# Kernel optimization log

Hardware: AMD Instinct MI355X
Metric: run time of the kernel (lower is better)

The kernel has to match this reference:

```python
import jax, jax.numpy as jnp
import numpy as np

NC = 80          # classes
REG_MAX = 16     # DFL bins
NK = 51          # 17*3 keypoint channels
KPT_SHAPE = (17, 3)
MAX_DET = 100
CONF_THRES = 0.25
STRIDES = (8, 16, 32)


def _conv1x1(f, w, b):
    # f: (B,C,H,W), w: (O,C), b: (O,) -> (B,O,H,W)
    return jnp.einsum('bchw,oc->bohw', f, w) + b[None, :, None, None]


def _make_anchors(shapes, strides, offset=0.5):
    pts, sts = [], []
    for (h, w), s in zip(shapes, strides):
        sx = jnp.arange(w, dtype=jnp.float32) + offset
        sy = jnp.arange(h, dtype=jnp.float32) + offset
        gy, gx = jnp.meshgrid(sy, sx, indexing='ij')
        pts.append(jnp.stack([gx, gy], -1).reshape(-1, 2))
        sts.append(jnp.full((h * w, 1), float(s), jnp.float32))
    # transposed as in _new_inference: anchors (2,A), strides (1,A)
    return jnp.concatenate(pts, 0).T, jnp.concatenate(sts, 0).T


def setup_inputs() -> dict:
    key = jax.random.key(0)
    ks = jax.random.split(key, 16)
    ch = (128, 256, 512)
    hw = ((80, 80), (40, 40), (20, 20))
    d = {}
    for i, (c, (h, w)) in enumerate(zip(ch, hw)):
        d[f'x{i}'] = jax.random.normal(ks[i], (16, c, h, w), jnp.float32)
    k = 3
    for name, oc in (('cv2', 4 * REG_MAX), ('cv3', NC), ('cv4', NK)):
        for i, c in enumerate(ch):
            d[f'{name}_w{i}'] = jax.random.normal(ks[k], (oc, c), jnp.float32) * 0.02
            d[f'{name}_b{i}'] = jnp.zeros((oc,), jnp.float32)
            k += 1
    return d


def reference(x0, x1, x2,
              cv2_w0, cv2_b0, cv2_w1, cv2_b1, cv2_w2, cv2_b2,
              cv3_w0, cv3_b0, cv3_w1, cv3_b1, cv3_w2, cv3_b2,
              cv4_w0, cv4_b0, cv4_w1, cv4_b1, cv4_w2, cv4_b2):
    feats = [x0, x1, x2]
    cv2 = [(cv2_w0, cv2_b0), (cv2_w1, cv2_b1), (cv2_w2, cv2_b2)]
    cv3 = [(cv3_w0, cv3_b0), (cv3_w1, cv3_b1), (cv3_w2, cv3_b2)]
    cv4 = [(cv4_w0, cv4_b0), (cv4_w1, cv4_b1), (cv4_w2, cv4_b2)]
    bs = x0.shape[0]

    # keypoint branch: cat over levels -> (bs, nk, A)
    kpt = jnp.concatenate(
        [_conv1x1(f, w, b).reshape(bs, NK, -1) for f, (w, b) in zip(feats, cv4)], -1)
    # box+cls branch -> (bs, 4*reg_max+nc, A)
    xcat = jnp.concatenate(
        [jnp.concatenate([_conv1x1(f, *cv2[i]), _conv1x1(f, *cv3[i])], 1).reshape(bs, 4 * REG_MAX + NC, -1)
         for i, f in enumerate(feats)], -1)
    box, cls = xcat[:, :4 * REG_MAX], xcat[:, 4 * REG_MAX:]

    shapes = [(f.shape[2], f.shape[3]) for f in feats]
    anchors, strides = _make_anchors(shapes, STRIDES)  # (2,A), (1,A)
    A = anchors.shape[1]

    # DFL decode: softmax over reg_max bins, expectation w/ arange weights
    p = jax.nn.softmax(box.reshape(bs, 4, REG_MAX, A), axis=2)
    dist = jnp.einsum('bfra,r->bfa', p, jnp.arange(REG_MAX, dtype=jnp.float32))
    lt, rb = dist[:, :2], dist[:, 2:]
    x1y1 = anchors[None] - lt
    x2y2 = anchors[None] + rb
    # xywh box coding, scaled by strides
    dbox = jnp.concatenate([(x1y1 + x2y2) * 0.5, x2y2 - x1y1], 1) * strides[None]  # (bs,4,A)

    # keypoint decode (Pose.kpts_decode, ndim==3)
    y = kpt.reshape(bs, KPT_SHAPE[0], KPT_SHAPE[1], A)
    kxy = (y[:, :, :2] * 2.0 + (anchors[None, None] - 0.5)) * strides[None, None]
    kv = jax.nn.sigmoid(y[:, :, 2:3])
    pred_kpts = jnp.concatenate([kxy, kv], 2).reshape(bs, NK, A).transpose(0, 2, 1)  # (bs,A,nk)

    # EfficientIdxNMS_TRT stand-in: sigmoid scores (score_activation=1),
    # class-agnostic deterministic top-k selection by best class score.
    scores = jax.nn.sigmoid(cls.transpose(0, 2, 1))  # (bs,A,nc)
    max_s = scores.max(-1)
    cls_id = jnp.argmax(scores, -1)
    top_s, top_i = jax.lax.top_k(max_s, MAX_DET)     # (bs,MAX_DET)
    num_dets = (top_s > CONF_THRES).sum(-1).astype(jnp.int32)[:, None]
    det_boxes = jnp.take_along_axis(dbox.transpose(0, 2, 1), top_i[..., None], 1)  # (bs,MAX_DET,4)
    det_classes = jnp.take_along_axis(cls_id, top_i, 1).astype(jnp.int32)
    # irregular keypoint gather via det indices (the pred_kpts[bs_indices, det_indices] step)
    det_kpts = jnp.take_along_axis(pred_kpts, top_i[..., None], 1).reshape(bs, MAX_DET, *KPT_SHAPE)
    return num_dets, det_boxes, top_s, det_classes, det_kpts
```

## Files before the change

kernel.cpp:

```cpp
#include <hip/hip_runtime.h>
#include <hip/hip_bf16.h>

#define NC 80
#define NK 51
#define REG_MAX 16
#define MAX_DET 100
#define A_TOT 8400
#define BS 16

#define OUT_NUM 0
#define OUT_BOX 16
#define OUT_SCORE (16 + 16*MAX_DET*4)
#define OUT_CLASS (OUT_SCORE + 16*MAX_DET)
#define OUT_KPT (OUT_CLASS + 16*MAX_DET)

static __device__ __forceinline__ unsigned long long mk_key(unsigned u, int a) {
    return ((unsigned long long)u << 32) | (unsigned)(0x7FFFFFFF - a);
}

__global__ __launch_bounds__(256) void scores_fused(
    const float* __restrict__ x0, const float* __restrict__ x1, const float* __restrict__ x2,
    const float* __restrict__ w0, const float* __restrict__ w1, const float* __restrict__ w2,
    const float* __restrict__ bias0, const float* __restrict__ bias1, const float* __restrict__ bias2,
    float* __restrict__ max_s,
    int* __restrict__ cls_id)
{
    __shared__ float fs[32 * 256];
    __shared__ float wsh[80 * 32];
    __shared__ float rm[4][256];
    __shared__ int   ri[4][256];

    int bid = blockIdx.x;
    const float *x, *w, *bias; int C, A, a_off, b, tile;
    if (bid < 32) {
        x = x2; w = w2; bias = bias2; C = 512; A = 400; a_off = 8000;
        b = bid >> 1; tile = bid & 1;
    } else if (bid < 144) {
        int r = bid - 32;
        x = x1; w = w1; bias = bias1; C = 256; A = 1600; a_off = 6400;
        b = r / 7; tile = r - b * 7;
    } else {
        int r = bid - 144;
        x = x0; w = w0; bias = bias0; C = 128; A = 6400; a_off = 0;
        b = r / 25; tile = r - b * 25;
    }
    int a0 = tile * 256;

    int t = threadIdx.x;
    int lane = t & 63;
    int wv = t >> 6;
    int oc0 = wv * 20;

    float acc[20][4];
#pragma unroll
    for (int j = 0; j < 20; ++j) {
        float bv = bias[oc0 + j];
        acc[j][0] = bv; acc[j][1] = bv; acc[j][2] = bv; acc[j][3] = bv;
    }

    const float* xb = x + (long)b * C * A;
    int nchunk = C >> 5;

    for (int kc = 0; kc < nchunk; ++kc) {
        __syncthreads();
#pragma unroll
        for (int i = 0; i < 8; ++i) {
            int idx = t + i * 256;
            int c = idx >> 6;
            int q = (idx & 63) * 4;
            int aa = a0 + q; if (aa > A - 4) aa = A - 4;
            float4 v = *(const float4*)(xb + (long)(kc * 32 + c) * A + aa);
            *(float4*)(&fs[c * 256 + q]) = v;
        }
#pragma unroll
        for (int i = 0; i < 3; ++i) {
            int idx = t + i * 256;
            if (idx < 640) {
                int oc = idx >> 3;
                int q = (idx & 7) * 4;
                float4 v = *(const float4*)(w + oc * C + kc * 32 + q);
                *(float4*)(&wsh[oc * 32 + q]) = v;
            }
        }
        __syncthreads();

#pragma unroll 1
        for (int c4 = 0; c4 < 32; c4 += 4) {
            float4 f[4];
#pragma unroll
            for (int cc = 0; cc < 4; ++cc)
                f[cc] = *(const float4*)(&fs[(c4 + cc) * 256 + lane * 4]);
#pragma unroll
            for (int j = 0; j < 20; ++j) {
                float4 w4 = *(const float4*)(&wsh[(oc0 + j) * 32 + c4]);
                acc[j][0] = fmaf(w4.x, f[0].x, acc[j][0]);
                acc[j][0] = fmaf(w4.y, f[1].x, acc[j][0]);
                acc[j][0] = fmaf(w4.z, f[2].x, acc[j][0]);
                acc[j][0] = fmaf(w4.w, f[3].x, acc[j][0]);
                acc[j][1] = fmaf(w4.x, f[0].y, acc[j][1]);
                acc[j][1] = fmaf(w4.y, f[1].y, acc[j][1]);
                acc[j][1] = fmaf(w4.z, f[2].y, acc[j][1]);
                acc[j][1] = fmaf(w4.w, f[3].y, acc[j][1]);
                acc[j][2] = fmaf(w4.x, f[0].z, acc[j][2]);
                acc[j][2] = fmaf(w4.y, f[1].z, acc[j][2]);
                acc[j][2] = fmaf(w4.z, f[2].z, acc[j][2]);
                acc[j][2] = fmaf(w4.w, f[3].z, acc[j][2]);
                acc[j][3] = fmaf(w4.x, f[0].w, acc[j][3]);
                acc[j][3] = fmaf(w4.y, f[1].w, acc[j][3]);
                acc[j][3] = fmaf(w4.z, f[2].w, acc[j][3]);
                acc[j][3] = fmaf(w4.w, f[3].w, acc[j][3]);
            }
        }
    }

#pragma unroll
    for (int q = 0; q < 4; ++q) {
        float m = acc[0][q]; int mi = 0;
#pragma unroll
        for (int j = 1; j < 20; ++j)
            if (acc[j][q] > m) { m = acc[j][q]; mi = j; }
        rm[wv][lane * 4 + q] = m;
        ri[wv][lane * 4 + q] = oc0 + mi;
    }
    __syncthreads();

    {
        float bm = rm[0][t]; int bi = ri[0][t];
#pragma unroll
        for (int v = 1; v < 4; ++v) {
            float om = rm[v][t];
            if (om > bm) { bm = om; bi = ri[v][t]; }
        }
        int ga = a0 + t;
        if (ga < A) {
            max_s[b * A_TOT + a_off + ga] = 1.0f / (1.0f + expf(-bm));
            cls_id[b * A_TOT + a_off + ga] = bi;
        }
    }
}

__global__ __launch_bounds__(256) void topk_kernel(
    const float* __restrict__ max_s,
    const int* __restrict__ cls_id,
    float* __restrict__ out,
    int* __restrict__ top_idx)
{
    int b = blockIdx.x;
    int t = threadIdx.x;
    int lane = t & 63;
    int wv = t >> 6;

    __shared__ unsigned hist[4 * 256];
    __shared__ int tieIdx[A_TOT];
    __shared__ unsigned long long highKeys[128];
    __shared__ unsigned long long finalKeys[128];
    __shared__ int wmin[4];
    __shared__ unsigned s_prefix;
    __shared__ int s_k, s_nHigh, s_nTie, s_cnt, s_bcast;

    uint4 uu[9];
#pragma unroll
    for (int i = 0; i < 9; ++i) {
        int idx = t + i * 256;
        if (i < 8 || t < 52)
            uu[i] = *(const uint4*)((const unsigned*)(max_s + (long)b * A_TOT) + idx * 4);
        else
            uu[i] = make_uint4(0u, 0u, 0u, 0u);
    }

    if (t == 0) { s_prefix = 0; s_k = MAX_DET; s_nHigh = 0; s_nTie = 0; s_cnt = 0; }

    for (int pass = 0; pass < 4; ++pass) {
#pragma unroll
        for (int j = 0; j < 4; ++j) hist[t + j * 256] = 0;
        __syncthreads();

        unsigned pre = s_prefix;
        int k = s_k;
        int shHi = 32 - 8 * pass;
        int shD = 24 - 8 * pass;
#pragma unroll
        for (int i = 0; i < 9; ++i) {
            if (i < 8 || t < 52) {
                unsigned e[4] = { uu[i].x, uu[i].y, uu[i].z, uu[i].w };
#pragma unroll
                for (int j = 0; j < 4; ++j) {
                    bool cand = (pass == 0) ? true : ((e[j] >> shHi) == pre);
                    if (cand)
                        atomicAdd(&hist[(wv << 8) + ((e[j] >> shD) & 0xFF)], 1u);
                }
            }
        }
        __syncthreads();

        if (wv == 0) {
            unsigned c0 = 0, c1 = 0, c2 = 0, c3 = 0;
#pragma unroll
            for (int w = 0; w < 4; ++w) {
                const unsigned* hp = &hist[(w << 8) + lane * 4];
                c0 += hp[0]; c1 += hp[1]; c2 += hp[2]; c3 += hp[3];
            }
            unsigned s3 = c3, s2 = c2 + s3, s1 = c1 + s2, s0 = c0 + s1;
            unsigned tsum = s0;
#pragma unroll
            for (int off = 1; off < 64; off <<= 1) {
                unsigned o = __shfl_down(tsum, off, 64);
                if (lane + off < 64) tsum += o;
            }
            unsigned excl = tsum - s0;
            unsigned S0 = excl + s0, S1 = excl + s1, S2 = excl + s2, S3 = excl + s3;
            int ld = -1;
            unsigned uk = (unsigned)k;
            if (S3 >= uk)      ld = lane * 4 + 3;
            else if (S2 >= uk) ld = lane * 4 + 2;
            else if (S1 >= uk) ld = lane * 4 + 1;
            else if (S0 >= uk) ld = lane * 4 + 0;
            int d = ld;
#pragma unroll
            for (int off = 32; off > 0; off >>= 1) d = max(d, __shfl_xor(d, off, 64));
            int dn = d + 1;
            unsigned mine = 0;
            if (dn < 256 && lane == (dn >> 2)) {
                int e = dn & 3;
                mine = (e == 0) ? S0 : (e == 1) ? S1 : (e == 2) ? S2 : S3;
            }
#pragma unroll
            for (int off = 32; off > 0; off >>= 1) mine += __shfl_xor(mine, off, 64);
            if (lane == 0) {
                s_k = k - (int)mine;
                s_prefix = (pre << 8) | (unsigned)d;
            }
        }
        __syncthreads();
    }

    unsigned cut = s_prefix;
    int r = s_k;

#pragma unroll
    for (int i = 0; i < 9; ++i) {
        if (i < 8 || t < 52) {
            unsigned e[4] = { uu[i].x, uu[i].y, uu[i].z, uu[i].w };
#pragma unroll
            for (int j = 0; j < 4; ++j) {
                int a = (t + i * 256) * 4 + j;
                if (e[j] > cut) {
                    int p = atomicAdd(&s_nHigh, 1);
                    highKeys[p] = mk_key(e[j], a);
                } else if (e[j] == cut) {
                    int p = atomicAdd(&s_nTie, 1);
                    tieIdx[p] = a;
                }
            }
        }
    }
    __syncthreads();
    int m = s_nHigh;
    int nt = s_nTie;

    if (t < 128) finalKeys[t] = 0ull;
    __syncthreads();
    if (t < m) finalKeys[t] = highKeys[t];

    if (nt == r) {
        if (t < nt) finalKeys[m + t] = mk_key(cut, tieIdx[t]);
        __syncthreads();
    } else {
        __syncthreads();
        for (int j = 0; j < r; ++j) {
            int mn = 0x7FFFFFFF;
            for (int p = t; p < nt; p += 256) mn = min(mn, tieIdx[p]);
            for (int off = 32; off > 0; off >>= 1) mn = min(mn, __shfl_down(mn, off, 64));
            if (lane == 0) wmin[wv] = mn;
            __syncthreads();
            if (t == 0) {
                int v = min(min(wmin[0], wmin[1]), min(wmin[2], wmin[3]));
                s_bcast = v;
                finalKeys[m + j] = mk_key(cut, v);
            }
            __syncthreads();
            int v = s_bcast;
            for (int p = t; p < nt; p += 256)
                if (tieIdx[p] == v) tieIdx[p] = 0x7FFFFFFF;
            __syncthreads();
        }
    }

    for (int ksz = 2; ksz <= 128; ksz <<= 1) {
        for (int j = ksz >> 1; j > 0; j >>= 1) {
            if (t < 128) {
                int ixj = t ^ j;
                if (ixj > t) {
                    bool desc = ((t & ksz) == 0);
                    unsigned long long x = finalKeys[t], y = finalKeys[ixj];
                    bool sw = desc ? (x < y) : (x > y);
                    if (sw) { finalKeys[t] = y; finalKeys[ixj] = x; }
                }
            }
            __syncthreads();
        }
    }

    if (t < MAX_DET) {
        unsigned long long kk = finalKeys[t];
        float sc = __uint_as_float((unsigned)(kk >> 32));
        int a = 0x7FFFFFFF - (int)(kk & 0xFFFFFFFFull);
        out[OUT_SCORE + b * MAX_DET + t] = sc;
        out[OUT_CLASS + b * MAX_DET + t] = (float)cls_id[b * A_TOT + a];
        top_idx[b * MAX_DET + t] = a;
        if (sc > 0.25f) atomicAdd(&s_cnt, 1);
    }
    __syncthreads();
    if (t == 0) out[OUT_NUM + b] = (float)s_cnt;
}

__global__ __launch_bounds__(128) void decode_kernel(
    const float* __restrict__ x0, const float* __restrict__ x1, const float* __restrict__ x2,
    const float* __restrict__ w2_0, const float* __restrict__ b2_0,
    const float* __restrict__ w2_1, const float* __restrict__ b2_1,
    const float* __restrict__ w2_2, const float* __restrict__ b2_2,
    const float* __restrict__ w4_0, const float* __restrict__ b4_0,
    const float* __restrict__ w4_1, const float* __restrict__ b4_1,
    const float* __restrict__ w4_2, const float* __restrict__ b4_2,
    const int* __restrict__ top_idx,
    float* __restrict__ out)
{
    int b = blockIdx.y;
    int k = blockIdx.x;
    int a = top_idx[b * MAX_DET + k];

    const float* x; const float* w2; const float* bb2; const float* w4; const float* bb4;
    int C, A, W, a_local; float stride;
    if (a < 6400)      { x = x0; C = 128; A = 6400; W = 80; stride = 8.0f;  a_local = a;        w2 = w2_0; bb2 = b2_0; w4 = w4_0; bb4 = b4_0; }
    else if (a < 8000) { x = x1; C = 256; A = 1600; W = 40; stride = 16.0f; a_local = a - 6400; w2 = w2_1; bb2 = b2_1; w4 = w4_1; bb4 = b4_1; }
    else               { x = x2; C = 512; A = 400;  W = 20; stride = 32.0f; a_local = a - 8000; w2 = w2_2; bb2 = b2_2; w4 = w4_2; bb4 = b4_2; }

    __shared__ float fs[512];
    __shared__ float logits[64];
    __shared__ float kraw[NK];
    __shared__ float dist[4];

    int t = threadIdx.x;
    for (int c = t; c < C; c += 128)
        fs[c] = x[((long)b * C + c) * A + a_local];
    __syncthreads();

    if (t < 64 + NK) {
        const float* wrow; float acc;
        if (t < 64) { wrow = w2 + t * C; acc = bb2[t]; }
        else        { wrow = w4 + (t - 64) * C; acc = bb4[t - 64]; }
        for (int c = 0; c < C; c += 4) {
            float4 wv4 = *(const float4*)(wrow + c);
            float4 fv4 = *(const float4*)(&fs[c]);
            acc = fmaf(wv4.x, fv4.x, acc);
            acc = fmaf(wv4.y, fv4.y, acc);
            acc = fmaf(wv4.z, fv4.z, acc);
            acc = fmaf(wv4.w, fv4.w, acc);
        }
        if (t < 64) logits[t] = acc;
        else        kraw[t - 64] = acc;
    }
    __syncthreads();

    if (t < 4) {
        float mx = logits[t * 16];
#pragma unroll
        for (int r = 1; r < 16; ++r) mx = fmaxf(mx, logits[t * 16 + r]);
        float se = 0.0f, sw = 0.0f;
#pragma unroll
        for (int r = 0; r < 16; ++r) {
            float e = expf(logits[t * 16 + r] - mx);
            se += e; sw += e * (float)r;
        }
        dist[t] = sw / se;
    }
    __syncthreads();

    float ax = (float)(a_local % W) + 0.5f;
    float ay = (float)(a_local / W) + 0.5f;

    if (t == 0) {
        float x1c = ax - dist[0], y1c = ay - dist[1];
        float x2c = ax + dist[2], y2c = ay + dist[3];
        float* ob = out + OUT_BOX + ((long)b * MAX_DET + k) * 4;
        ob[0] = (x1c + x2c) * 0.5f * stride;
        ob[1] = (y1c + y2c) * 0.5f * stride;
        ob[2] = (x2c - x1c) * stride;
        ob[3] = (y2c - y1c) * stride;
    }
    if (t < 17) {
        float vx = kraw[t * 3], vy = kraw[t * 3 + 1], vv = kraw[t * 3 + 2];
        float gx = ax - 0.5f, gy = ay - 0.5f;
        float* ok = out + OUT_KPT + (((long)b * MAX_DET + k) * 17 + t) * 3;
        ok[0] = (vx * 2.0f + gx) * stride;
        ok[1] = (vy * 2.0f + gy) * stride;
        ok[2] = 1.0f / (1.0f + expf(-vv));
    }
}

extern "C" void kernel_launch(void* const* d_in, const int* in_sizes, int n_in,
                              void* d_out, int out_size, void* d_ws, size_t ws_size,
                              hipStream_t stream) {
    const float* x0 = (const float*)d_in[0];
    const float* x1 = (const float*)d_in[1];
    const float* x2 = (const float*)d_in[2];
    const float* w2[3] = {(const float*)d_in[3], (const float*)d_in[5], (const float*)d_in[7]};
    const float* b2[3] = {(const float*)d_in[4], (const float*)d_in[6], (const float*)d_in[8]};
    const float* w3[3] = {(const float*)d_in[9], (const float*)d_in[11], (const float*)d_in[13]};
    const float* b3[3] = {(const float*)d_in[10], (const float*)d_in[12], (const float*)d_in[14]};
    const float* w4[3] = {(const float*)d_in[15], (const float*)d_in[17], (const float*)d_in[19]};
    const float* b4[3] = {(const float*)d_in[16], (const float*)d_in[18], (const float*)d_in[20]};

    float* out = (float*)d_out;

    float* ws_maxs = (float*)d_ws;
    int* ws_cls = (int*)(ws_maxs + BS * A_TOT);
    int* ws_top = (int*)(ws_cls + BS * A_TOT);

    scores_fused<<<dim3(544), 256, 0, stream>>>(
        x0, x1, x2, w3[0], w3[1], w3[2], b3[0], b3[1], b3[2], ws_maxs, ws_cls);
    topk_kernel<<<dim3(BS), 256, 0, stream>>>(ws_maxs, ws_cls, out, ws_top);
    decode_kernel<<<dim3(MAX_DET, BS), 128, 0, stream>>>(
        x0, x1, x2,
        w2[0], b2[0], w2[1], b2[1], w2[2], b2[2],
        w4[0], b4[0], w4[1], b4[1], w4[2], b4[2],
        ws_top, out);
}
```

Baseline: 311.4 us.

## Split output-channel work across blocks for deep pyramid levels to balance load

The class-score GEMM for levels 1 and 2 is now split across output-channel groups: four blocks of 20 channels for level 2 and two blocks of 40 for level 1. Each group writes a partial max and argmax to workspace, and the topk kernel merges them before selection. This targets load imbalance, where a few blocks looped over 512 channels and left the GPU underfilled at the tail. In exchange the deeper levels reload the feature tiles once per channel group, and the serial topk kernel gains a merge pass. The kernel is also templated on channel count so loops unroll at compile time.

```diff
diff --git a/kernel.cpp b/kernel.cpp
--- a/kernel.cpp
+++ b/kernel.cpp
@@ -18,48 +18,32 @@
     return ((unsigned long long)u << 32) | (unsigned)(0x7FFFFFFF - a);
 }
 
-__global__ __launch_bounds__(256) void scores_fused(
-    const float* __restrict__ x0, const float* __restrict__ x1, const float* __restrict__ x2,
-    const float* __restrict__ w0, const float* __restrict__ w1, const float* __restrict__ w2,
-    const float* __restrict__ bias0, const float* __restrict__ bias1, const float* __restrict__ bias2,
-    float* __restrict__ max_s,
-    int* __restrict__ cls_id)
+template<int C, int NOC>
+static __device__ __forceinline__ void score_tile(
+    const float* __restrict__ x, const float* __restrict__ w,
+    const float* __restrict__ bias,
+    int b, int a0, int oc_base, int A,
+    float* __restrict__ out_m, int* __restrict__ out_i,
+    float* __restrict__ fs, float* __restrict__ wsh,
+    float (*rm)[256], int (*ri)[256])
 {
-    __shared__ float fs[32 * 256];
-    __shared__ float wsh[80 * 32];
-    __shared__ float rm[4][256];
-    __shared__ int   ri[4][256];
-
-    int bid = blockIdx.x;
-    const float *x, *w, *bias; int C, A, a_off, b, tile;
-    if (bid < 32) {
-        x = x2; w = w2; bias = bias2; C = 512; A = 400; a_off = 8000;
-        b = bid >> 1; tile = bid & 1;
-    } else if (bid < 144) {
-        int r = bid - 32;
-        x = x1; w = w1; bias = bias1; C = 256; A = 1600; a_off = 6400;
-        b = r / 7; tile = r - b * 7;
-    } else {
-        int r = bid - 144;
-        x = x0; w = w0; bias = bias0; C = 128; A = 6400; a_off = 0;
-        b = r / 25; tile = r - b * 25;
-    }
-    int a0 = tile * 256;
+    constexpr int O = NOC / 4;
+    constexpr int NF4 = NOC * 8;
 
     int t = threadIdx.x;
     int lane = t & 63;
     int wv = t >> 6;
-    int oc0 = wv * 20;
-
-    float acc[20][4];
-#pragma unroll
-    for (int j = 0; j < 20; ++j) {
-        float bv = bias[oc0 + j];
+    int oc0 = wv * O;
+
+    float acc[O][4];
+#pragma unroll
+    for (int j = 0; j < O; ++j) {
+        float bv = bias[oc_base + oc0 + j];
         acc[j][0] = bv; acc[j][1] = bv; acc[j][2] = bv; acc[j][3] = bv;
     }
 
     const float* xb = x + (long)b * C * A;
-    int nchunk = C >> 5;
+    constexpr int nchunk = C >> 5;
 
     for (int kc = 0; kc < nchunk; ++kc) {
         __syncthreads();
@@ -75,10 +59,10 @@
 #pragma unroll
         for (int i = 0; i < 3; ++i) {
             int idx = t + i * 256;
-            if (idx < 640) {
+            if (idx < NF4) {
                 int oc = idx >> 3;
                 int q = (idx & 7) * 4;
-                float4 v = *(const float4*)(w + oc * C + kc * 32 + q);
+                float4 v = *(const float4*)(w + (long)(oc_base + oc) * C + kc * 32 + q);
                 *(float4*)(&wsh[oc * 32 + q]) = v;
             }
         }
@@ -91,7 +75,7 @@
             for (int cc = 0; cc < 4; ++cc)
                 f[cc] = *(const float4*)(&fs[(c4 + cc) * 256 + lane * 4]);
 #pragma unroll
-            for (int j = 0; j < 20; ++j) {
+            for (int j = 0; j < O; ++j) {
                 float4 w4 = *(const float4*)(&wsh[(oc0 + j) * 32 + c4]);
                 acc[j][0] = fmaf(w4.x, f[0].x, acc[j][0]);
                 acc[j][0] = fmaf(w4.y, f[1].x, acc[j][0]);
@@ -117,10 +101,10 @@
     for (int q = 0; q < 4; ++q) {
         float m = acc[0][q]; int mi = 0;
 #pragma unroll
-        for (int j = 1; j < 20; ++j)
+        for (int j = 1; j < O; ++j)
             if (acc[j][q] > m) { m = acc[j][q]; mi = j; }
         rm[wv][lane * 4 + q] = m;
-        ri[wv][lane * 4 + q] = oc0 + mi;
+        ri[wv][lane * 4 + q] = oc_base + oc0 + mi;
     }
     __syncthreads();
 
@@ -133,15 +117,55 @@
         }
         int ga = a0 + t;
         if (ga < A) {
-            max_s[b * A_TOT + a_off + ga] = 1.0f / (1.0f + expf(-bm));
-            cls_id[b * A_TOT + a_off + ga] = bi;
-        }
+            out_m[ga] = 1.0f / (1.0f + expf(-bm));
+            out_i[ga] = bi;
+        }
+    }
+}
+
+__global__ __launch_bounds__(256) void scores_fused(
+    const float* __restrict__ x0, const float* __restrict__ x1, const float* __restrict__ x2,
+    const float* __restrict__ w0, const float* __restrict__ w1, const float* __restrict__ w2,
+    const float* __restrict__ bias0, const float* __restrict__ bias1, const float* __restrict__ bias2,
+    float* __restrict__ max_s,
+    int* __restrict__ cls_id,
+    float* __restrict__ l1m, int* __restrict__ l1i,
+    float* __restrict__ l2m, int* __restrict__ l2i)
+{
+    __shared__ float fs[32 * 256];
+    __shared__ float wsh[80 * 32];
+    __shared__ float rm[4][256];
+    __shared__ int   ri[4][256];
+
+    int bid = blockIdx.x;
+    if (bid < 128) {
+        int b = bid >> 3, rem = bid & 7;
+        int tile = rem >> 2, g = rem & 3;
+        float* om; int* oi;
+        if (g == 0) { om = max_s + (long)b * A_TOT + 8000; oi = cls_id + (long)b * A_TOT + 8000; }
+        else        { om = l2m + ((long)(g - 1) * BS + b) * 400; oi = l2i + ((long)(g - 1) * BS + b) * 400; }
+        score_tile<512, 20>(x2, w2, bias2, b, tile * 256, g * 20, 400, om, oi, fs, wsh, rm, ri);
+    } else if (bid < 352) {
+        int r = bid - 128;
+        int b = r / 14, rem = r - b * 14;
+        int tile = rem >> 1, g = rem & 1;
+        float* om; int* oi;
+        if (g == 0) { om = max_s + (long)b * A_TOT + 6400; oi = cls_id + (long)b * A_TOT + 6400; }
+        else        { om = l1m + (long)b * 1600; oi = l1i + (long)b * 1600; }
+        score_tile<256, 40>(x1, w1, bias1, b, tile * 256, g * 40, 1600, om, oi, fs, wsh, rm, ri);
+    } else {
+        int r = bid - 352;
+        int b = r / 25, tile = r - b * 25;
+        score_tile<128, 80>(x0, w0, bias0, b, tile * 256, 0, 6400,
+            max_s + (long)b * A_TOT, cls_id + (long)b * A_TOT, fs, wsh, rm, ri);
     }
 }
 
 __global__ __launch_bounds__(256) void topk_kernel(
-    const float* __restrict__ max_s,
-    const int* __restrict__ cls_id,
+    float* __restrict__ max_s,
+    int* __restrict__ cls_id,
+    const float* __restrict__ l1m, const int* __restrict__ l1i,
+    const float* __restrict__ l2m, const int* __restrict__ l2i,
     float* __restrict__ out,
     int* __restrict__ top_idx)
 {
@@ -149,6 +173,27 @@
     int t = threadIdx.x;
     int lane = t & 63;
     int wv = t >> 6;
+
+    for (int a = t; a < 1600; a += 256) {
+        float bs_ = max_s[(long)b * A_TOT + 6400 + a];
+        int   bi_ = cls_id[(long)b * A_TOT + 6400 + a];
+        float s1 = l1m[(long)b * 1600 + a];
+        if (s1 > bs_) { bs_ = s1; bi_ = l1i[(long)b * 1600 + a]; }
+        max_s[(long)b * A_TOT + 6400 + a] = bs_;
+        cls_id[(long)b * A_TOT + 6400 + a] = bi_;
+    }
+    for (int a = t; a < 400; a += 256) {
+        float bs_ = max_s[(long)b * A_TOT + 8000 + a];
+        int   bi_ = cls_id[(long)b * A_TOT + 8000 + a];
+#pragma unroll
+        for (int g = 0; g < 3; ++g) {
+            float s = l2m[((long)g * BS + b) * 400 + a];
+            if (s > bs_) { bs_ = s; bi_ = l2i[((long)g * BS + b) * 400 + a]; }
+        }
+        max_s[(long)b * A_TOT + 8000 + a] = bs_;
+        cls_id[(long)b * A_TOT + 8000 + a] = bi_;
+    }
+    __syncthreads();
 
     __shared__ unsigned hist[4 * 256];
     __shared__ int tieIdx[A_TOT];
@@ -414,12 +459,18 @@
     float* out = (float*)d_out;
 
     float* ws_maxs = (float*)d_ws;
-    int* ws_cls = (int*)(ws_maxs + BS * A_TOT);
-    int* ws_top = (int*)(ws_cls + BS * A_TOT);
-
-    scores_fused<<<dim3(544), 256, 0, stream>>>(
-        x0, x1, x2, w3[0], w3[1], w3[2], b3[0], b3[1], b3[2], ws_maxs, ws_cls);
-    topk_kernel<<<dim3(BS), 256, 0, stream>>>(ws_maxs, ws_cls, out, ws_top);
+    int*   ws_cls  = (int*)(ws_maxs + BS * A_TOT);
+    int*   ws_top  = (int*)(ws_cls + BS * A_TOT);
+    float* ws_l1m  = (float*)(ws_top + BS * MAX_DET);
+    int*   ws_l1i  = (int*)(ws_l1m + BS * 1600);
+    float* ws_l2m  = (float*)(ws_l1i + BS * 1600);
+    int*   ws_l2i  = (int*)(ws_l2m + 3 * BS * 400);
+
+    scores_fused<<<dim3(752), 256, 0, stream>>>(
+        x0, x1, x2, w3[0], w3[1], w3[2], b3[0], b3[1], b3[2],
+        ws_maxs, ws_cls, ws_l1m, ws_l1i, ws_l2m, ws_l2i);
+    topk_kernel<<<dim3(BS), 256, 0, stream>>>(
+        ws_maxs, ws_cls, ws_l1m, ws_l1i, ws_l2m, ws_l2i, out, ws_top);
     decode_kernel<<<dim3(MAX_DET, BS), 128, 0, stream>>>(
         x0, x1, x2,
         w2[0], b2[0], w2[1], b2[1], w2[2], b2[2],
```

Measured after the change: 303.3 us. 1.03x faster.
